# Optimization experiments

Measured on AMD Instinct MI355X. Metric: run time of the kernel, lower is better.

The kernel has to match this reference:

```python
import jax, jax.numpy as jnp
import numpy as np

IN_FEATURES = 1024
OUT_FEATURES = 1024
N_LEAF = 16
BATCH = 4096


def setup_inputs() -> dict:
    key = jax.random.key(0)
    k_x, k_gw, k_pw = jax.random.split(key, 3)
    x = jax.random.normal(k_x, (BATCH, IN_FEATURES), dtype=jnp.float32)
    # xavier_normal for gating weights [in, L]
    gw_std = np.sqrt(2.0 / (IN_FEATURES + N_LEAF))
    gw = jax.random.normal(k_gw, (IN_FEATURES, N_LEAF), dtype=jnp.float32) * gw_std
    gb = jnp.zeros((N_LEAF,), dtype=jnp.float32)
    # kaiming_normal (linear) on [out*L, in] then reshaped to [out, in, L]
    pw_std = np.sqrt(1.0 / IN_FEATURES)
    pw = jax.random.normal(k_pw, (OUT_FEATURES, IN_FEATURES, N_LEAF), dtype=jnp.float32) * pw_std
    pb = jnp.zeros((OUT_FEATURES, N_LEAF), dtype=jnp.float32)
    return {"x": x, "gw": gw, "gb": gb, "pw": pw, "pb": pb}


def reference(x, gw, gb, pw, pb):
    # gatings: softmax over leaves, [B, L]
    g = jax.nn.softmax(x @ gw + gb, axis=1)
    # Fused contraction order (same math as materializing per-sample [out,in]
    # projection matrices): per-leaf projections then gating-weighted sum.
    # leaf_out[b,o,l] = sum_i x[b,i] * pw[o,i,l]
    leaf_out = jnp.einsum('bi,oil->bol', x, pw)
    # result[b,o] = sum_l leaf_out[b,o,l] * g[b,l] + sum_l pb[o,l] * g[b,l]
    result = jnp.einsum('bol,bl->bo', leaf_out, g) + g @ pb.T
    return result
```

## Files before the change

### kernel.cpp

```cpp
#include <hip/hip_runtime.h>
#include <hip/hip_bf16.h>
#include <stdint.h>

#define IN_F   1024
#define OUT_F  1024
#define NLEAF  16
#define BATCH  4096

#define KK      1024
#define NN      (OUT_F * NLEAF)
#define TM      128
#define TN      128
#define BK      32
#define KITERS  (KK / BK)
#define GS_PAD  138

typedef __bf16 bf16x8 __attribute__((ext_vector_type(8)));
typedef float  f32x4  __attribute__((ext_vector_type(4)));

#define ASYNC_COPY16(gp, lp)                                                         \
  __builtin_amdgcn_global_load_lds((const __attribute__((address_space(1))) void*)(gp), \
                                   (__attribute__((address_space(3))) void*)(lp),       \
                                   16, 0, 0)

__global__ __launch_bounds__(256) void gate_pack_kernel(
    const float* __restrict__ x, const float* __restrict__ gw,
    const float* __restrict__ gb, float* __restrict__ g,
    __hip_bfloat16* __restrict__ xb) {
  const int lane = threadIdx.x & 63;
  const int wv   = threadIdx.x >> 6;
  const int b    = blockIdx.x * 4 + wv;
  const int i4   = lane >> 4;
  const int l    = lane & 15;

  const float* xrow = x + (size_t)b * IN_F;
  float acc = 0.f;
#pragma unroll 8
  for (int k = 0; k < IN_F / 4; ++k) {
    const float xv = xrow[k * 4 + i4];
    const float wvv = gw[k * 64 + lane];
    acc = fmaf(xv, wvv, acc);
  }
  acc += __shfl_xor(acc, 16);
  acc += __shfl_xor(acc, 32);
  float logit = acc + gb[l];
  float m = logit;
#pragma unroll
  for (int off = 8; off > 0; off >>= 1) m = fmaxf(m, __shfl_xor(m, off));
  float e = __expf(logit - m);
  float s = e;
#pragma unroll
  for (int off = 8; off > 0; off >>= 1) s += __shfl_xor(s, off);
  if (lane < NLEAF) g[b * NLEAF + l] = e / s;

  const float* xblk = x + (size_t)blockIdx.x * 4 * IN_F;
  __hip_bfloat16* xbblk = xb + (size_t)blockIdx.x * 4 * IN_F;
#pragma unroll
  for (int j = 0; j < 2; ++j) {
    const int f = (threadIdx.x + 256 * j) * 8;
    const float4 a0 = *(const float4*)(xblk + f);
    const float4 a1 = *(const float4*)(xblk + f + 4);
    __align__(16) __hip_bfloat16 tmp[8];
    tmp[0] = __float2bfloat16(a0.x); tmp[1] = __float2bfloat16(a0.y);
    tmp[2] = __float2bfloat16(a0.z); tmp[3] = __float2bfloat16(a0.w);
    tmp[4] = __float2bfloat16(a1.x); tmp[5] = __float2bfloat16(a1.y);
    tmp[6] = __float2bfloat16(a1.z); tmp[7] = __float2bfloat16(a1.w);
    *(uint4*)(xbblk + f) = *(const uint4*)tmp;
  }
}

__global__ __launch_bounds__(256) void pack_w_kernel(
    const float* __restrict__ pw, __hip_bfloat16* __restrict__ W) {
  __shared__ __align__(16) __hip_bfloat16 lt[16 * 264];
  const int o = blockIdx.x;
  const int t = threadIdx.x;
  const float* src = pw + (size_t)o * (IN_F * NLEAF);

  for (int ch = 0; ch < 4; ++ch) {
    const float4* p = (const float4*)(src + ch * 4096 + t * 16);
    const float4 v0 = p[0], v1 = p[1], v2 = p[2], v3 = p[3];
    if (ch) __syncthreads();
    lt[ 0 * 264 + t] = __float2bfloat16(v0.x);
    lt[ 1 * 264 + t] = __float2bfloat16(v0.y);
    lt[ 2 * 264 + t] = __float2bfloat16(v0.z);
    lt[ 3 * 264 + t] = __float2bfloat16(v0.w);
    lt[ 4 * 264 + t] = __float2bfloat16(v1.x);
    lt[ 5 * 264 + t] = __float2bfloat16(v1.y);
    lt[ 6 * 264 + t] = __float2bfloat16(v1.z);
    lt[ 7 * 264 + t] = __float2bfloat16(v1.w);
    lt[ 8 * 264 + t] = __float2bfloat16(v2.x);
    lt[ 9 * 264 + t] = __float2bfloat16(v2.y);
    lt[10 * 264 + t] = __float2bfloat16(v2.z);
    lt[11 * 264 + t] = __float2bfloat16(v2.w);
    lt[12 * 264 + t] = __float2bfloat16(v3.x);
    lt[13 * 264 + t] = __float2bfloat16(v3.y);
    lt[14 * 264 + t] = __float2bfloat16(v3.z);
    lt[15 * 264 + t] = __float2bfloat16(v3.w);
    __syncthreads();
#pragma unroll
    for (int jj = 0; jj < 2; ++jj) {
      const int u = t + 256 * jj;
      const int l = u >> 5;
      const int i8 = (u & 31) * 8;
      *(uint4*)(W + ((size_t)o * NLEAF + l) * KK + ch * 256 + i8) =
          *(const uint4*)(lt + l * 264 + i8);
    }
  }
}

__global__ __launch_bounds__(256, 2) void gemm_kernel(
    const __hip_bfloat16* __restrict__ Xb,
    const __hip_bfloat16* __restrict__ W,
    const float* __restrict__ g,
    const float* __restrict__ pb,
    float* __restrict__ out) {
  __shared__ __align__(16) __hip_bfloat16 As[TM * BK];
  __shared__ __align__(16) __hip_bfloat16 Bs[TN * BK];
  __shared__ float gs[NLEAF * GS_PAD];
  __shared__ float pbs[8 * NLEAF];

  const int t    = threadIdx.x;
  const int lane = t & 63;
  const int w    = t >> 6;
  const int quad = lane >> 4;
  const int r16  = lane & 15;

  const int b0 = blockIdx.x * TN;
  const int n0 = blockIdx.y * TM;

  const __hip_bfloat16* aG = W + (long)n0 * KK;
  const __hip_bfloat16* bG = Xb + (long)b0 * KK;

#pragma unroll
  for (int j = 0; j < 8; ++j) {
    const int f = t + 256 * j;
    gs[(f & 15) * GS_PAD + (f >> 4)] = g[b0 * NLEAF + f];
  }
  if (t < 128) pbs[t] = pb[n0 + t];

  const int  c0 = t, c1 = t + 256;
  const int  sl0 = (c0 & 3) ^ ((c0 >> 3) & 3);
  const int  sl1 = (c1 & 3) ^ ((c1 >> 3) & 3);
  const long aOff0 = (long)(c0 >> 2) * KK + sl0 * 8;
  const long aOff1 = (long)(c1 >> 2) * KK + sl1 * 8;

  const int wn = (w >> 1) * 64;
  const int wb = (w & 1) * 64;
  const int swz = (r16 >> 1) & 3;

  f32x4 acc[4][4] = {};

  for (int it = 0; it < KITERS; ++it) {
    ASYNC_COPY16(aG + aOff0, (char*)As + c0 * 16);
    ASYNC_COPY16(aG + aOff1, (char*)As + c1 * 16);
    ASYNC_COPY16(bG + aOff0, (char*)Bs + c0 * 16);
    ASYNC_COPY16(bG + aOff1, (char*)Bs + c1 * 16);
    __syncthreads();

    bf16x8 af[4], bfr[4];
#pragma unroll
    for (int mi = 0; mi < 4; ++mi)
      af[mi] = *(const bf16x8*)(As + (wn + mi * 16 + r16) * BK + (quad ^ swz) * 8);
#pragma unroll
    for (int ni = 0; ni < 4; ++ni)
      bfr[ni] = *(const bf16x8*)(Bs + (wb + ni * 16 + r16) * BK + (quad ^ swz) * 8);

#pragma unroll
    for (int mi = 0; mi < 4; ++mi)
#pragma unroll
      for (int ni = 0; ni < 4; ++ni)
        acc[mi][ni] = __builtin_amdgcn_mfma_f32_16x16x32_bf16(
            af[mi], bfr[ni], acc[mi][ni], 0, 0, 0);

    __syncthreads();
    aG += BK;
    bG += BK;
  }

  float pbv[4][4];
#pragma unroll
  for (int mi = 0; mi < 4; ++mi)
#pragma unroll
    for (int r = 0; r < 4; ++r)
      pbv[mi][r] = pbs[((wn >> 4) + mi) * NLEAF + quad * 4 + r];

  const int oBase = (n0 >> 4) + (wn >> 4);
#pragma unroll
  for (int ni = 0; ni < 4; ++ni) {
    const int bl = wb + ni * 16 + r16;
    float gv[4];
#pragma unroll
    for (int r = 0; r < 4; ++r) gv[r] = gs[(quad * 4 + r) * GS_PAD + bl];
    float rv[4];
#pragma unroll
    for (int mi = 0; mi < 4; ++mi) {
      float v = 0.f;
#pragma unroll
      for (int r = 0; r < 4; ++r)
        v = fmaf(acc[mi][ni][r] + pbv[mi][r], gv[r], v);
      v += __shfl_xor(v, 16);
      v += __shfl_xor(v, 32);
      rv[mi] = v;
    }
    if (quad == 0)
      *(float4*)(out + (long)(b0 + bl) * OUT_F + oBase) =
          make_float4(rv[0], rv[1], rv[2], rv[3]);
  }
}

__global__ __launch_bounds__(256) void gate_kernel_fb(
    const float* __restrict__ x, const float* __restrict__ gw,
    const float* __restrict__ gb, float* __restrict__ g) {
  const int lane = threadIdx.x & 63;
  const int wv   = threadIdx.x >> 6;
  const int b    = blockIdx.x * 4 + wv;
  const int i4   = lane >> 4;
  const int l    = lane & 15;
  const float* xrow = x + (size_t)b * IN_F;
  float acc = 0.f;
  for (int k = 0; k < IN_F / 4; ++k)
    acc = fmaf(xrow[k * 4 + i4], gw[k * 64 + lane], acc);
  acc += __shfl_xor(acc, 16);
  acc += __shfl_xor(acc, 32);
  float logit = acc + gb[l];
  float m = logit;
  for (int off = 8; off > 0; off >>= 1) m = fmaxf(m, __shfl_xor(m, off));
  float e = __expf(logit - m);
  float s = e;
  for (int off = 8; off > 0; off >>= 1) s += __shfl_xor(s, off);
  if (lane < NLEAF) g[b * NLEAF + l] = e / s;
}

__global__ __launch_bounds__(256) void fallback_kernel(
    const float* __restrict__ x, const float* __restrict__ pw,
    const float* __restrict__ pb, const float* __restrict__ g,
    float* __restrict__ out) {
  const int b = blockIdx.x;
  __shared__ float xs[IN_F];
  __shared__ float gsl[NLEAF];
  const int t = threadIdx.x;
  for (int j = t; j < IN_F; j += 256) xs[j] = x[(long)b * IN_F + j];
  if (t < NLEAF) gsl[t] = g[b * NLEAF + t];
  __syncthreads();
  for (int o = t; o < OUT_F; o += 256) {
    const float* pwo = pw + (long)o * (IN_F * NLEAF);
    float acc = 0.f;
    for (int i = 0; i < IN_F; ++i) {
      const float xv = xs[i];
      float wsum = 0.f;
#pragma unroll
      for (int l = 0; l < NLEAF; ++l) wsum += gsl[l] * pwo[i * NLEAF + l];
      acc += xv * wsum;
    }
    float bias = 0.f;
#pragma unroll
    for (int l = 0; l < NLEAF; ++l) bias += gsl[l] * pb[o * NLEAF + l];
    out[(long)b * OUT_F + o] = acc + bias;
  }
}

extern "C" void kernel_launch(void* const* d_in, const int* in_sizes, int n_in,
                              void* d_out, int out_size, void* d_ws, size_t ws_size,
                              hipStream_t stream) {
  const float* x  = (const float*)d_in[0];
  const float* gw = (const float*)d_in[1];
  const float* gb = (const float*)d_in[2];
  const float* pw = (const float*)d_in[3];
  const float* pb = (const float*)d_in[4];
  float* out = (float*)d_out;

  const size_t w_bytes  = (size_t)NN * KK * sizeof(__hip_bfloat16);
  const size_t xb_bytes = (size_t)BATCH * KK * sizeof(__hip_bfloat16);
  const size_t g_bytes  = (size_t)BATCH * NLEAF * sizeof(float);

  if (ws_size >= w_bytes + xb_bytes + g_bytes) {
    __hip_bfloat16* W  = (__hip_bfloat16*)d_ws;
    __hip_bfloat16* xb = (__hip_bfloat16*)((char*)d_ws + w_bytes);
    float*          g  = (float*)((char*)d_ws + w_bytes + xb_bytes);

    gate_pack_kernel<<<BATCH / 4, 256, 0, stream>>>(x, gw, gb, g, xb);
    pack_w_kernel<<<OUT_F, 256, 0, stream>>>(pw, W);
    gemm_kernel<<<dim3(BATCH / TN, NN / TM), 256, 0, stream>>>(xb, W, g, pb, out);
  } else {
    float* g = (float*)d_ws;
    gate_kernel_fb<<<BATCH / 4, 256, 0, stream>>>(x, gw, gb, g);
    fallback_kernel<<<BATCH, 256, 0, stream>>>(x, pw, pb, g, out);
  }
}
```

Before: 286.2 us.

## Merge prep kernels and alias GEMM epilogue smem to raise occupancy

Merges the gate/x-pack kernel and the weight-pack kernel into one launch, with the block index choosing the branch, which removes one launch and lets both workloads share the GPU. In the GEMM, the gating and bias shared buffers now alias the A/B tile region and are loaded after the main loop, which cuts LDS per block, and launch bounds are raised to 4 blocks per CU. The main risks are register spilling under the tighter launch bound, and the extra post-loop sync and global loads added to the epilogue.

```diff
diff --git a/kernel.cpp b/kernel.cpp
--- a/kernel.cpp
+++ b/kernel.cpp
@@ -23,101 +23,103 @@
                                    (__attribute__((address_space(3))) void*)(lp),       \
                                    16, 0, 0)
 
-__global__ __launch_bounds__(256) void gate_pack_kernel(
+__global__ __launch_bounds__(256) void prep_kernel(
     const float* __restrict__ x, const float* __restrict__ gw,
-    const float* __restrict__ gb, float* __restrict__ g,
-    __hip_bfloat16* __restrict__ xb) {
-  const int lane = threadIdx.x & 63;
-  const int wv   = threadIdx.x >> 6;
-  const int b    = blockIdx.x * 4 + wv;
-  const int i4   = lane >> 4;
-  const int l    = lane & 15;
-
-  const float* xrow = x + (size_t)b * IN_F;
-  float acc = 0.f;
+    const float* __restrict__ gb, const float* __restrict__ pw,
+    float* __restrict__ g, __hip_bfloat16* __restrict__ xb,
+    __hip_bfloat16* __restrict__ W) {
+  __shared__ __align__(16) __hip_bfloat16 lt[16 * 264];
+  const int t = threadIdx.x;
+
+  if (blockIdx.x < OUT_F) {
+    const int o = blockIdx.x;
+    const float* src = pw + (size_t)o * (IN_F * NLEAF);
+    for (int ch = 0; ch < 4; ++ch) {
+      const float4* p = (const float4*)(src + ch * 4096 + t * 16);
+      const float4 v0 = p[0], v1 = p[1], v2 = p[2], v3 = p[3];
+      if (ch) __syncthreads();
+      lt[ 0 * 264 + t] = __float2bfloat16(v0.x);
+      lt[ 1 * 264 + t] = __float2bfloat16(v0.y);
+      lt[ 2 * 264 + t] = __float2bfloat16(v0.z);
+      lt[ 3 * 264 + t] = __float2bfloat16(v0.w);
+      lt[ 4 * 264 + t] = __float2bfloat16(v1.x);
+      lt[ 5 * 264 + t] = __float2bfloat16(v1.y);
+      lt[ 6 * 264 + t] = __float2bfloat16(v1.z);
+      lt[ 7 * 264 + t] = __float2bfloat16(v1.w);
+      lt[ 8 * 264 + t] = __float2bfloat16(v2.x);
+      lt[ 9 * 264 + t] = __float2bfloat16(v2.y);
+      lt[10 * 264 + t] = __float2bfloat16(v2.z);
+      lt[11 * 264 + t] = __float2bfloat16(v2.w);
+      lt[12 * 264 + t] = __float2bfloat16(v3.x);
+      lt[13 * 264 + t] = __float2bfloat16(v3.y);
+      lt[14 * 264 + t] = __float2bfloat16(v3.z);
+      lt[15 * 264 + t] = __float2bfloat16(v3.w);
+      __syncthreads();
+#pragma unroll
+      for (int jj = 0; jj < 2; ++jj) {
+        const int u = t + 256 * jj;
+        const int l = u >> 5;
+        const int i8 = (u & 31) * 8;
+        *(uint4*)(W + ((size_t)o * NLEAF + l) * KK + ch * 256 + i8) =
+            *(const uint4*)(lt + l * 264 + i8);
+      }
+    }
+  } else {
+    const int blk  = blockIdx.x - OUT_F;
+    const int lane = t & 63;
+    const int wv   = t >> 6;
+    const int b    = blk * 4 + wv;
+    const int i4   = lane >> 4;
+    const int l    = lane & 15;
+
+    const float* xrow = x + (size_t)b * IN_F;
+    float acc = 0.f;
 #pragma unroll 8
-  for (int k = 0; k < IN_F / 4; ++k) {
-    const float xv = xrow[k * 4 + i4];
-    const float wvv = gw[k * 64 + lane];
-    acc = fmaf(xv, wvv, acc);
-  }
-  acc += __shfl_xor(acc, 16);
-  acc += __shfl_xor(acc, 32);
-  float logit = acc + gb[l];
-  float m = logit;
-#pragma unroll
-  for (int off = 8; off > 0; off >>= 1) m = fmaxf(m, __shfl_xor(m, off));
-  float e = __expf(logit - m);
-  float s = e;
-#pragma unroll
-  for (int off = 8; off > 0; off >>= 1) s += __shfl_xor(s, off);
-  if (lane < NLEAF) g[b * NLEAF + l] = e / s;
-
-  const float* xblk = x + (size_t)blockIdx.x * 4 * IN_F;
-  __hip_bfloat16* xbblk = xb + (size_t)blockIdx.x * 4 * IN_F;
-#pragma unroll
-  for (int j = 0; j < 2; ++j) {
-    const int f = (threadIdx.x + 256 * j) * 8;
-    const float4 a0 = *(const float4*)(xblk + f);
-    const float4 a1 = *(const float4*)(xblk + f + 4);
-    __align__(16) __hip_bfloat16 tmp[8];
-    tmp[0] = __float2bfloat16(a0.x); tmp[1] = __float2bfloat16(a0.y);
-    tmp[2] = __float2bfloat16(a0.z); tmp[3] = __float2bfloat16(a0.w);
-    tmp[4] = __float2bfloat16(a1.x); tmp[5] = __float2bfloat16(a1.y);
-    tmp[6] = __float2bfloat16(a1.z); tmp[7] = __float2bfloat16(a1.w);
-    *(uint4*)(xbblk + f) = *(const uint4*)tmp;
-  }
-}
-
-__global__ __launch_bounds__(256) void pack_w_kernel(
-    const float* __restrict__ pw, __hip_bfloat16* __restrict__ W) {
-  __shared__ __align__(16) __hip_bfloat16 lt[16 * 264];
-  const int o = blockIdx.x;
-  const int t = threadIdx.x;
-  const float* src = pw + (size_t)o * (IN_F * NLEAF);
-
-  for (int ch = 0; ch < 4; ++ch) {
-    const float4* p = (const float4*)(src + ch * 4096 + t * 16);
-    const float4 v0 = p[0], v1 = p[1], v2 = p[2], v3 = p[3];
-    if (ch) __syncthreads();
-    lt[ 0 * 264 + t] = __float2bfloat16(v0.x);
-    lt[ 1 * 264 + t] = __float2bfloat16(v0.y);
-    lt[ 2 * 264 + t] = __float2bfloat16(v0.z);
-    lt[ 3 * 264 + t] = __float2bfloat16(v0.w);
-    lt[ 4 * 264 + t] = __float2bfloat16(v1.x);
-    lt[ 5 * 264 + t] = __float2bfloat16(v1.y);
-    lt[ 6 * 264 + t] = __float2bfloat16(v1.z);
-    lt[ 7 * 264 + t] = __float2bfloat16(v1.w);
-    lt[ 8 * 264 + t] = __float2bfloat16(v2.x);
-    lt[ 9 * 264 + t] = __float2bfloat16(v2.y);
-    lt[10 * 264 + t] = __float2bfloat16(v2.z);
-    lt[11 * 264 + t] = __float2bfloat16(v2.w);
-    lt[12 * 264 + t] = __float2bfloat16(v3.x);
-    lt[13 * 264 + t] = __float2bfloat16(v3.y);
-    lt[14 * 264 + t] = __float2bfloat16(v3.z);
-    lt[15 * 264 + t] = __float2bfloat16(v3.w);
-    __syncthreads();
-#pragma unroll
-    for (int jj = 0; jj < 2; ++jj) {
-      const int u = t + 256 * jj;
-      const int l = u >> 5;
-      const int i8 = (u & 31) * 8;
-      *(uint4*)(W + ((size_t)o * NLEAF + l) * KK + ch * 256 + i8) =
-          *(const uint4*)(lt + l * 264 + i8);
-    }
-  }
-}
-
-__global__ __launch_bounds__(256, 2) void gemm_kernel(
+    for (int k = 0; k < IN_F / 4; ++k) {
+      const float xv = xrow[k * 4 + i4];
+      const float wvv = gw[k * 64 + lane];
+      acc = fmaf(xv, wvv, acc);
+    }
+    acc += __shfl_xor(acc, 16);
+    acc += __shfl_xor(acc, 32);
+    float logit = acc + gb[l];
+    float m = logit;
+#pragma unroll
+    for (int off = 8; off > 0; off >>= 1) m = fmaxf(m, __shfl_xor(m, off));
+    float e = __expf(logit - m);
+    float s = e;
+#pragma unroll
+    for (int off = 8; off > 0; off >>= 1) s += __shfl_xor(s, off);
+    if (lane < NLEAF) g[b * NLEAF + l] = e / s;
+
+    const float* xblk = x + (size_t)blk * 4 * IN_F;
+    __hip_bfloat16* xbblk = xb + (size_t)blk * 4 * IN_F;
+#pragma unroll
+    for (int j = 0; j < 2; ++j) {
+      const int f = (t + 256 * j) * 8;
+      const float4 a0 = *(const float4*)(xblk + f);
+      const float4 a1 = *(const float4*)(xblk + f + 4);
+      __align__(16) __hip_bfloat16 tmp[8];
+      tmp[0] = __float2bfloat16(a0.x); tmp[1] = __float2bfloat16(a0.y);
+      tmp[2] = __float2bfloat16(a0.z); tmp[3] = __float2bfloat16(a0.w);
+      tmp[4] = __float2bfloat16(a1.x); tmp[5] = __float2bfloat16(a1.y);
+      tmp[6] = __float2bfloat16(a1.z); tmp[7] = __float2bfloat16(a1.w);
+      *(uint4*)(xbblk + f) = *(const uint4*)tmp;
+    }
+  }
+}
+
+__global__ __launch_bounds__(256, 4) void gemm_kernel(
     const __hip_bfloat16* __restrict__ Xb,
     const __hip_bfloat16* __restrict__ W,
     const float* __restrict__ g,
     const float* __restrict__ pb,
     float* __restrict__ out) {
-  __shared__ __align__(16) __hip_bfloat16 As[TM * BK];
-  __shared__ __align__(16) __hip_bfloat16 Bs[TN * BK];
-  __shared__ float gs[NLEAF * GS_PAD];
-  __shared__ float pbs[8 * NLEAF];
+  __shared__ __align__(16) char smem[16384];
+  __hip_bfloat16* As = (__hip_bfloat16*)smem;
+  __hip_bfloat16* Bs = (__hip_bfloat16*)(smem + 8192);
+  float* gs  = (float*)smem;
+  float* pbs = (float*)(smem + 8832);
 
   const int t    = threadIdx.x;
   const int lane = t & 63;
@@ -130,13 +132,6 @@
 
   const __hip_bfloat16* aG = W + (long)n0 * KK;
   const __hip_bfloat16* bG = Xb + (long)b0 * KK;
-
-#pragma unroll
-  for (int j = 0; j < 8; ++j) {
-    const int f = t + 256 * j;
-    gs[(f & 15) * GS_PAD + (f >> 4)] = g[b0 * NLEAF + f];
-  }
-  if (t < 128) pbs[t] = pb[n0 + t];
 
   const int  c0 = t, c1 = t + 256;
   const int  sl0 = (c0 & 3) ^ ((c0 >> 3) & 3);
@@ -176,6 +171,14 @@
     aG += BK;
     bG += BK;
   }
+
+#pragma unroll
+  for (int j = 0; j < 8; ++j) {
+    const int f = t + 256 * j;
+    gs[(f & 15) * GS_PAD + (f >> 4)] = g[b0 * NLEAF + f];
+  }
+  if (t < 128) pbs[t] = pb[n0 + t];
+  __syncthreads();
 
   float pbv[4][4];
 #pragma unroll
@@ -278,8 +281,7 @@
     __hip_bfloat16* xb = (__hip_bfloat16*)((char*)d_ws + w_bytes);
     float*          g  = (float*)((char*)d_ws + w_bytes + xb_bytes);
 
-    gate_pack_kernel<<<BATCH / 4, 256, 0, stream>>>(x, gw, gb, g, xb);
-    pack_w_kernel<<<OUT_F, 256, 0, stream>>>(pw, W);
+    prep_kernel<<<OUT_F + BATCH / 4, 256, 0, stream>>>(x, gw, gb, pw, g, xb, W);
     gemm_kernel<<<dim3(BATCH / TN, NN / TM), 256, 0, stream>>>(xb, W, g, pb, out);
   } else {
     float* g = (float*)d_ws;
```

Result: no change. 283.5 us (-0.9%).
